# Kernel tuning notes

Measured on AMD Instinct MI355X. Metric: run time of the kernel, lower is better.

The kernel has to match this reference:

```python
import jax, jax.numpy as jnp
import numpy as np

B, S, D, V, L = 64, 2048, 256, 256, 4


def setup_inputs() -> dict:
    key = jax.random.key(0)
    ks = jax.random.split(key, 8)
    s = 1.0 / np.sqrt(D)  # PyTorch GRU init scale
    return {
        "x": jax.random.randint(ks[0], (B, S), 0, V, dtype=jnp.int32),
        "emb": jax.random.normal(ks[1], (V, D), jnp.float32) * 0.02,
        "W_ih": jax.random.uniform(ks[2], (L, 3 * D, D), jnp.float32, -s, s),
        "W_hh": jax.random.uniform(ks[3], (L, 3 * D, D), jnp.float32, -s, s),
        "b_ih": jax.random.uniform(ks[4], (L, 3 * D), jnp.float32, -s, s),
        "b_hh": jax.random.uniform(ks[5], (L, 3 * D), jnp.float32, -s, s),
        "W_out": jax.random.uniform(ks[6], (V, D), jnp.float32, -s, s),
        "b_out": jax.random.uniform(ks[7], (V,), jnp.float32, -s, s),
    }


def _gru_layer(seq, Wi, Wh, bi, bh):
    # seq: [B, S, D]. Precompute input-side gates for all timesteps (one GEMM).
    gi_all = jnp.einsum("bsd,gd->bsg", seq, Wi) + bi  # [B, S, 3D]

    def step(h, gi):
        gh = h @ Wh.T + bh  # [B, 3D]
        i_r, i_z, i_n = jnp.split(gi, 3, axis=-1)
        h_r, h_z, h_n = jnp.split(gh, 3, axis=-1)
        r = jax.nn.sigmoid(i_r + h_r)
        z = jax.nn.sigmoid(i_z + h_z)
        n = jnp.tanh(i_n + r * h_n)
        h_new = (1.0 - z) * n + z * h
        return h_new, h_new

    h0 = jnp.zeros((seq.shape[0], Wh.shape[1]), seq.dtype)
    _, out_t = jax.lax.scan(step, h0, jnp.swapaxes(gi_all, 0, 1))  # [S, B, D]
    return jnp.swapaxes(out_t, 0, 1)


def reference(x, emb, W_ih, W_hh, b_ih, b_hh, W_out, b_out):
    seq = emb[x]  # [B, S, D] embedding gather
    for l in range(W_ih.shape[0]):  # fixed small layer loop
        seq = _gru_layer(seq, W_ih[l], W_hh[l], b_ih[l], b_hh[l])
    logits = jnp.einsum("bsd,vd->bsv", seq, W_out) + b_out  # [B, S, V]
    return logits
```

## Files before the change

### kernel.cpp

```cpp
#include <hip/hip_runtime.h>
#include <hip/hip_bf16.h>


#define B_ 64
#define S_ 2048
#define D_ 256
#define V_ 256
#define L_ 4

typedef short  s16x8 __attribute__((ext_vector_type(8)));
typedef float  f32x4 __attribute__((ext_vector_type(4)));

static __device__ __forceinline__ unsigned short f2b(float f){
  union { float f; unsigned int u; } v; v.f = f;
  unsigned int u = v.u;
  return (unsigned short)((u + 0x7FFFu + ((u >> 16) & 1u)) >> 16);
}
static __device__ __forceinline__ float b2f_lo(unsigned int u){
  union { unsigned int u; float f; } v; v.u = u << 16; return v.f;
}
static __device__ __forceinline__ float b2f_hi(unsigned int u){
  union { unsigned int u; float f; } v; v.u = u & 0xffff0000u; return v.f;
}

static __device__ __forceinline__ void lds_load16(void* lds, const void* g){
  __builtin_amdgcn_global_load_lds(
      (const __attribute__((address_space(1))) unsigned int*)g,
      (__attribute__((address_space(3))) unsigned int*)lds, 16, 0, 0);
}

__global__ void cast_bf16_kernel(const float* __restrict__ src,
                                 unsigned short* __restrict__ dst, int n){
  int i = blockIdx.x * 256 + threadIdx.x;
  if (i < n) dst[i] = f2b(src[i]);
}

__global__ void embed_kernel(const int* __restrict__ x, const float* __restrict__ emb,
                             unsigned short* __restrict__ seq){
  int bs = blockIdx.x;
  int d  = threadIdx.x;
  int tok = x[bs];
  seq[(size_t)bs * D_ + d] = f2b(emb[tok * D_ + d]);
}

template<int OUTF32>
__global__ __launch_bounds__(256) void gemm_bt(const unsigned short* __restrict__ A,
                                               const unsigned short* __restrict__ Bw,
                                               const float* __restrict__ bias,
                                               void* __restrict__ Cp,
                                               int M, int N, int K, int ldc){
  __shared__ __align__(16) unsigned short As[128 * 32];
  __shared__ __align__(16) unsigned short Bs[128 * 32];
  const int tid = threadIdx.x, lane = tid & 63, w = tid >> 6;
  const int col = lane & 15, q = lane >> 4;
  const int m0 = blockIdx.x * 128, n0 = blockIdx.y * 128;
  const int mW = (w & 1) * 64, nW = (w >> 1) * 64;
  const size_t rowb = (size_t)K * 2;

  f32x4 acc[4][4] = {};

  for (int k0 = 0; k0 < K; k0 += 32){
    __syncthreads();
    #pragma unroll
    for (int inst = 0; inst < 2; ++inst){
      int c = inst * 256 + w * 64 + lane;
      int row = c >> 2, c16 = c & 3;
      lds_load16((char*)As + (inst * 4096 + w * 1024),
                 (const char*)A  + (size_t)(m0 + row) * rowb + (size_t)k0 * 2 + c16 * 16);
      lds_load16((char*)Bs + (inst * 4096 + w * 1024),
                 (const char*)Bw + (size_t)(n0 + row) * rowb + (size_t)k0 * 2 + c16 * 16);
    }
    __syncthreads();
    s16x8 aF[4], bF[4];
    #pragma unroll
    for (int t = 0; t < 4; ++t){
      aF[t] = *(const s16x8*)&As[(mW + t * 16 + col) * 32 + q * 8];
      bF[t] = *(const s16x8*)&Bs[(nW + t * 16 + col) * 32 + q * 8];
    }
    #pragma unroll
    for (int mi = 0; mi < 4; ++mi)
      #pragma unroll
      for (int ni = 0; ni < 4; ++ni)
        acc[mi][ni] = __builtin_amdgcn_mfma_f32_16x16x32_bf16(aF[mi], bF[ni], acc[mi][ni], 0, 0, 0);
  }

  float bn[4];
  #pragma unroll
  for (int ni = 0; ni < 4; ++ni) bn[ni] = bias[n0 + nW + ni * 16 + col];

  if (OUTF32){
    #pragma unroll
    for (int mi = 0; mi < 4; ++mi)
      #pragma unroll
      for (int ni = 0; ni < 4; ++ni)
        #pragma unroll
        for (int i = 0; i < 4; ++i){
          int r  = m0 + mW + mi * 16 + 4 * q + i;
          int cN = n0 + nW + ni * 16 + col;
          ((float*)Cp)[(size_t)r * ldc + cN] = acc[mi][ni][i] + bn[ni];
        }
  } else {
    const int b     = m0 >> 11;
    const int bi    = b >> 2;
    const int qs    = b & 3;
    const int sbase = (m0 & 2047) + mW;
    #pragma unroll
    for (int mi = 0; mi < 4; ++mi)
      #pragma unroll
      for (int ni = 0; ni < 4; ++ni)
        #pragma unroll
        for (int i = 0; i < 4; ++i){
          int s  = sbase + mi * 16 + 4 * q + i;
          int cN = n0 + nW + ni * 16 + col;
          int g  = cN >> 8, d = cN & 255;
          int lane_s = (d >> 5) * 64 + qs * 16 + (d & 15);
          int j  = ((d >> 4) & 1) * 3 + g;
          float v = acc[mi][ni][i] + bn[ni];
          size_t us = ((size_t)((bi * 2048 + s) * 3 + (j >> 1)) * 512 + lane_s) * 2 + (j & 1);
          ((unsigned short*)Cp)[us] = f2b(v);
        }
  }
}

__global__ __launch_bounds__(512, 2) void gru_scan(const unsigned int* __restrict__ gi32,
                                                   const unsigned short* __restrict__ Wh,
                                                   const float* __restrict__ bh,
                                                   unsigned short* __restrict__ outp){
  __shared__ __align__(16) unsigned short hb[2][4096];
  const int tid = threadIdx.x, lane = tid & 63, w = tid >> 6;
  const int col = lane & 15, q = lane >> 4;
  const int bi = blockIdx.x;
  const int dbase = w * 32;

  s16x8 bw[6][8];
  float bhv[6];
  #pragma unroll
  for (int g = 0; g < 3; ++g)
    #pragma unroll
    for (int t2 = 0; t2 < 2; ++t2){
      int gcol = g * 256 + dbase + t2 * 16 + col;
      bhv[g * 2 + t2] = bh[gcol];
      #pragma unroll
      for (int kk = 0; kk < 8; ++kk)
        bw[g * 2 + t2][kk] = *(const s16x8*)(Wh + gcol * 256 + kk * 32 + q * 8);
    }

  for (int i = tid; i < 4096; i += 512){ hb[0][i] = 0; hb[1][i] = 0; }

  float hprev[2] = {0.f, 0.f};
  const size_t obase = (size_t)(bi * 4 + q) * (S_ * D_) + dbase + col;

  const unsigned int* gp = gi32 + (size_t)bi * (S_ * 1536) + (w * 64 + lane);
  unsigned int cA0 = gp[0], cA1 = gp[512], cA2 = gp[1024];

  __syncthreads();

  auto step = [&](const unsigned short* hcur, unsigned short* hnxt,
                  unsigned int c0, unsigned int c1, unsigned int c2, int sidx){
    f32x4 acc[6];
    #pragma unroll
    for (int t = 0; t < 6; ++t){ f32x4 vv = {bhv[t], bhv[t], bhv[t], bhv[t]}; acc[t] = vv; }
    s16x8 a0 = *(const s16x8*)&hcur[lane * 8];
    #pragma unroll
    for (int kk = 0; kk < 8; ++kk){
      s16x8 aN = a0;
      if (kk < 7) aN = *(const s16x8*)&hcur[(kk + 1) * 512 + lane * 8];
      #pragma unroll
      for (int t = 0; t < 6; ++t)
        acc[t] = __builtin_amdgcn_mfma_f32_16x16x32_bf16(a0, bw[t][kk], acc[t], 0, 0, 0);
      a0 = aN;
    }
    float giR[2] = { b2f_lo(c0), b2f_hi(c1) };
    float giZ[2] = { b2f_hi(c0), b2f_lo(c2) };
    float giN[2] = { b2f_lo(c1), b2f_hi(c2) };
    #pragma unroll
    for (int t2 = 0; t2 < 2; ++t2){
      const int d = dbase + t2 * 16 + col;
      float pr = acc[t2][0]     + giR[t2];
      float pz = acc[2 + t2][0] + giZ[t2];
      float rg = __builtin_amdgcn_rcpf(1.f + __expf(-pr));
      float zg = __builtin_amdgcn_rcpf(1.f + __expf(-pz));
      float na = giN[t2] + rg * acc[4 + t2][0];
      float e2 = __expf(2.f * na);
      float ng = 1.f - 2.f * __builtin_amdgcn_rcpf(e2 + 1.f);
      float hn = ng + zg * (hprev[t2] - ng);
      hprev[t2] = hn;
      unsigned short hbits = f2b(hn);
      outp[obase + (size_t)sidx * D_ + t2 * 16] = hbits;
      hnxt[(d >> 5) * 512 + ((4 * q) + 16 * ((d >> 3) & 3)) * 8 + (d & 7)] = hbits;
    }
    asm volatile("s_waitcnt lgkmcnt(0)" ::: "memory");
    __builtin_amdgcn_s_barrier();
    asm volatile("" ::: "memory");
  };

  unsigned int cB0, cB1, cB2;
  for (int s = 0; s < S_; s += 2){
    cB0 = gp[1536]; cB1 = gp[1536 + 512]; cB2 = gp[1536 + 1024];
    step(hb[0], hb[1], cA0, cA1, cA2, s);
    const unsigned int* gpn = (s + 2 < S_) ? (gp + 3072) : gp;
    cA0 = gpn[0]; cA1 = gpn[512]; cA2 = gpn[1024];
    step(hb[1], hb[0], cB0, cB1, cB2, s + 1);
    gp += 3072;
  }
}

extern "C" void kernel_launch(void* const* d_in, const int* in_sizes, int n_in,
                              void* d_out, int out_size, void* d_ws, size_t ws_size,
                              hipStream_t stream){
  const int*   x    = (const int*)  d_in[0];
  const float* emb  = (const float*)d_in[1];
  const float* Wih  = (const float*)d_in[2];
  const float* Whh  = (const float*)d_in[3];
  const float* bih  = (const float*)d_in[4];
  const float* bhh  = (const float*)d_in[5];
  const float* Wout = (const float*)d_in[6];
  const float* bout = (const float*)d_in[7];
  float* out = (float*)d_out;

  char* ws = (char*)d_ws;
  unsigned short* seqA  = (unsigned short*)(ws);
  unsigned short* seqB  = (unsigned short*)(ws +  67108864);
  unsigned short* gibuf = (unsigned short*)(ws + 134217728);
  unsigned short* wihB  = (unsigned short*)(ws + 335544320);
  unsigned short* whhB  = (unsigned short*)(ws + 337117184);
  unsigned short* woutB = (unsigned short*)(ws + 338690048);

  cast_bf16_kernel<<<3072, 256, 0, stream>>>(Wih,  wihB,  L_ * 768 * 256);
  cast_bf16_kernel<<<3072, 256, 0, stream>>>(Whh,  whhB,  L_ * 768 * 256);
  cast_bf16_kernel<<< 256, 256, 0, stream>>>(Wout, woutB, V_ * D_);
  embed_kernel<<<B_ * S_, 256, 0, stream>>>(x, emb, seqA);

  const int M = B_ * S_;
  unsigned short* sIn = seqA;
  unsigned short* sOut = seqB;
  for (int l = 0; l < L_; ++l){
    gemm_bt<0><<<dim3(M / 128, 6), 256, 0, stream>>>(sIn, wihB + (size_t)l * 768 * 256,
                                                     bih + l * 768, gibuf, M, 768, 256, 768);
    gru_scan<<<16, 512, 0, stream>>>((const unsigned int*)gibuf,
                                     whhB + (size_t)l * 768 * 256, bhh + l * 768, sOut);
    unsigned short* t = sIn; sIn = sOut; sOut = t;
  }
  gemm_bt<1><<<dim3(M / 128, 2), 256, 0, stream>>>(sIn, woutB, bout, out, M, 256, 256, 256);
}
```

Measured before the change: 8.922 ms.

## Fuse all GRU layers into one persistent wavefront-pipelined kernel with flag sync

```diff
diff --git a/kernel.cpp b/kernel.cpp
--- a/kernel.cpp
+++ b/kernel.cpp
@@ -7,6 +7,11 @@
 #define D_ 256
 #define V_ 256
 #define L_ 4
+#define CHUNK_ 64
+#define NCHUNK_ 32
+#define LAG_ 2
+#define NWORK_ 192
+#define SLOTDW_ (16 * 64 * 1536)
 
 typedef short  s16x8 __attribute__((ext_vector_type(8)));
 typedef float  f32x4 __attribute__((ext_vector_type(4)));
@@ -27,6 +32,24 @@
   __builtin_amdgcn_global_load_lds(
       (const __attribute__((address_space(1))) unsigned int*)g,
       (__attribute__((address_space(3))) unsigned int*)lds, 16, 0, 0);
+}
+
+static __device__ __forceinline__ int aload(const int* p){
+  return __hip_atomic_load(p, __ATOMIC_RELAXED, __HIP_MEMORY_SCOPE_AGENT);
+}
+static __device__ __forceinline__ void spin_ge(const int* p, int tgt){
+  int n = 0;
+  while (aload(p) < tgt && n < 4000000){ __builtin_amdgcn_s_sleep(32); ++n; }
+}
+static __device__ __forceinline__ void spin_min16_ge(const int* p, int tgt){
+  int n = 0;
+  for (;;){
+    int m = 0x7fffffff;
+    #pragma unroll
+    for (int i = 0; i < 16; ++i) m = min(m, aload(p + i));
+    if (m >= tgt || n > 4000000) break;
+    __builtin_amdgcn_s_sleep(32); ++n;
+  }
 }
 
 __global__ void cast_bf16_kernel(const float* __restrict__ src,
@@ -43,12 +66,189 @@
   seq[(size_t)bs * D_ + d] = f2b(emb[tok * D_ + d]);
 }
 
-template<int OUTF32>
-__global__ __launch_bounds__(256) void gemm_bt(const unsigned short* __restrict__ A,
-                                               const unsigned short* __restrict__ Bw,
-                                               const float* __restrict__ bias,
-                                               void* __restrict__ Cp,
-                                               int M, int N, int K, int ldc){
+__global__ void init_flags_kernel(int* flags){
+  int i = threadIdx.x;
+  if (i < 192) flags[i] = 0;
+}
+
+__global__ __launch_bounds__(512, 2) void gru_pipe(
+    unsigned short* bufA, unsigned short* bufB,
+    unsigned int* ring,
+    const unsigned short* wih, const unsigned short* whh,
+    const float* bih, const float* bhh,
+    int* flags)
+{
+  __shared__ __align__(16) unsigned short smem[8192];
+  const int blk = blockIdx.x;
+  const int tid = threadIdx.x, lane = tid & 63, w = tid >> 6;
+  const int col = lane & 15, q = lane >> 4;
+  int* scanprog = flags;
+  int* jobdone  = flags + 64;
+
+  if (blk < 64){
+    const int l = blk >> 4, bi = blk & 15;
+    const unsigned short* Wh = whh + (size_t)l * 768 * 256;
+    const float* bh = bhh + l * 768;
+    unsigned short* outp = (l & 1) ? bufA : bufB;
+    const unsigned int* ringL = ring + (size_t)l * 2 * SLOTDW_;
+    const int dbase = w * 32;
+
+    s16x8 bw[6][8];
+    float bhv[6];
+    #pragma unroll
+    for (int g = 0; g < 3; ++g)
+      #pragma unroll
+      for (int t2 = 0; t2 < 2; ++t2){
+        int gcol = g * 256 + dbase + t2 * 16 + col;
+        bhv[g * 2 + t2] = bh[gcol];
+        #pragma unroll
+        for (int kk = 0; kk < 8; ++kk)
+          bw[g * 2 + t2][kk] = *(const s16x8*)(Wh + gcol * 256 + kk * 32 + q * 8);
+      }
+
+    unsigned short* hb0 = smem;
+    unsigned short* hb1 = smem + 4096;
+    for (int i = tid; i < 8192; i += 512) smem[i] = 0;
+
+    float hprev[2] = {0.f, 0.f};
+    const size_t obase = (size_t)(bi * 4 + q) * (S_ * D_) + dbase + col;
+    __syncthreads();
+
+    auto step = [&](const unsigned short* hcur, unsigned short* hnxt,
+                    unsigned int c0, unsigned int c1, unsigned int c2, int sidx){
+      f32x4 acc[6];
+      #pragma unroll
+      for (int t = 0; t < 6; ++t){ f32x4 vv = {bhv[t], bhv[t], bhv[t], bhv[t]}; acc[t] = vv; }
+      s16x8 a0 = *(const s16x8*)&hcur[lane * 8];
+      #pragma unroll
+      for (int kk = 0; kk < 8; ++kk){
+        s16x8 aN = a0;
+        if (kk < 7) aN = *(const s16x8*)&hcur[(kk + 1) * 512 + lane * 8];
+        #pragma unroll
+        for (int t = 0; t < 6; ++t)
+          acc[t] = __builtin_amdgcn_mfma_f32_16x16x32_bf16(a0, bw[t][kk], acc[t], 0, 0, 0);
+        a0 = aN;
+      }
+      float giR[2] = { b2f_lo(c0), b2f_hi(c1) };
+      float giZ[2] = { b2f_hi(c0), b2f_lo(c2) };
+      float giN[2] = { b2f_lo(c1), b2f_hi(c2) };
+      #pragma unroll
+      for (int t2 = 0; t2 < 2; ++t2){
+        const int d = dbase + t2 * 16 + col;
+        float pr = acc[t2][0]     + giR[t2];
+        float pz = acc[2 + t2][0] + giZ[t2];
+        float rg = __builtin_amdgcn_rcpf(1.f + __expf(-pr));
+        float zg = __builtin_amdgcn_rcpf(1.f + __expf(-pz));
+        float na = giN[t2] + rg * acc[4 + t2][0];
+        float e2 = __expf(2.f * na);
+        float ng = 1.f - 2.f * __builtin_amdgcn_rcpf(e2 + 1.f);
+        float hn = ng + zg * (hprev[t2] - ng);
+        hprev[t2] = hn;
+        unsigned short hbits = f2b(hn);
+        outp[obase + (size_t)sidx * D_ + t2 * 16] = hbits;
+        hnxt[(d >> 5) * 512 + ((4 * q) + 16 * ((d >> 3) & 3)) * 8 + (d & 7)] = hbits;
+      }
+      asm volatile("s_waitcnt lgkmcnt(0)" ::: "memory");
+      __builtin_amdgcn_s_barrier();
+      asm volatile("" ::: "memory");
+    };
+
+    for (int c = 0; c < NCHUNK_; ++c){
+      if (tid == 0) spin_ge(&jobdone[l * 32 + c], NWORK_);
+      __syncthreads();
+      __threadfence();
+      const unsigned int* gp = ringL + (size_t)(c & 1) * SLOTDW_ + bi * (64 * 1536) + (w * 64 + lane);
+      unsigned int cA0 = gp[0], cA1 = gp[512], cA2 = gp[1024];
+      const int sg0 = c * 64;
+      for (int s2 = 0; s2 < 64; s2 += 2){
+        const unsigned int* gq = gp + (size_t)(s2 + 1) * 1536;
+        unsigned int cB0 = gq[0], cB1 = gq[512], cB2 = gq[1024];
+        step(hb0, hb1, cA0, cA1, cA2, sg0 + s2);
+        const unsigned int* gr = gp + (size_t)((s2 + 2 < 64) ? s2 + 2 : s2) * 1536;
+        cA0 = gr[0]; cA1 = gr[512]; cA2 = gr[1024];
+        step(hb1, hb0, cB0, cB1, cB2, sg0 + s2 + 1);
+      }
+      __syncthreads();
+      __threadfence();
+      if (tid == 0)
+        __hip_atomic_store(&scanprog[l * 16 + bi], c + 1, __ATOMIC_RELAXED, __HIP_MEMORY_SCOPE_AGENT);
+    }
+  } else {
+    const int W = blk - 64, jm = W / 6, jn = W % 6;
+    unsigned short* As = smem;
+    unsigned short* Bs = smem + 4096;
+    const int mW = (w & 1) * 64, nW = (w >> 1) * 32;
+    const int rr = tid >> 2, c16 = tid & 3;
+
+    for (int T = 0; T <= NCHUNK_ - 1 + 3 * LAG_; ++T){
+      for (int l = 0; l < 4; ++l){
+        const int c = T - l * LAG_;
+        if (c < 0 || c >= NCHUNK_) continue;
+        if (tid == 0){
+          spin_min16_ge(&scanprog[l * 16], c - 1);
+          if (l > 0) spin_min16_ge(&scanprog[(l - 1) * 16], c + 1);
+        }
+        __syncthreads();
+        __threadfence();
+
+        const unsigned short* inA = (l & 1) ? bufB : bufA;
+        const unsigned short* Bw  = wih + (size_t)l * 768 * 256;
+        const float* bias = bih + l * 768;
+        const unsigned short* Arow = inA
+            + ((size_t)(2 * jm + (rr >> 6)) * S_ + (size_t)c * 64 + (rr & 63)) * 256;
+        const unsigned short* Brow = Bw + (size_t)(jn * 128 + rr) * 256;
+
+        f32x4 acc[4][2] = {};
+        for (int k0 = 0; k0 < 256; k0 += 32){
+          __syncthreads();
+          lds_load16((char*)As + tid * 16, (const char*)Arow + k0 * 2 + c16 * 16);
+          lds_load16((char*)Bs + tid * 16, (const char*)Brow + k0 * 2 + c16 * 16);
+          __syncthreads();
+          s16x8 aF[4], bF[2];
+          #pragma unroll
+          for (int t = 0; t < 4; ++t) aF[t] = *(const s16x8*)&As[(mW + t * 16 + col) * 32 + q * 8];
+          #pragma unroll
+          for (int t = 0; t < 2; ++t) bF[t] = *(const s16x8*)&Bs[(nW + t * 16 + col) * 32 + q * 8];
+          #pragma unroll
+          for (int mi = 0; mi < 4; ++mi)
+            #pragma unroll
+            for (int ni = 0; ni < 2; ++ni)
+              acc[mi][ni] = __builtin_amdgcn_mfma_f32_16x16x32_bf16(aF[mi], bF[ni], acc[mi][ni], 0, 0, 0);
+        }
+        float bn[2];
+        #pragma unroll
+        for (int ni = 0; ni < 2; ++ni) bn[ni] = bias[jn * 128 + nW + ni * 16 + col];
+
+        const int b = 2 * jm + (mW >> 6), bi2 = b >> 2, qs = b & 3;
+        unsigned short* slotB = (unsigned short*)(ring + (size_t)(l * 2 + (c & 1)) * SLOTDW_);
+        #pragma unroll
+        for (int mi = 0; mi < 4; ++mi)
+          #pragma unroll
+          for (int ni = 0; ni < 2; ++ni)
+            #pragma unroll
+            for (int i = 0; i < 4; ++i){
+              int sL = mi * 16 + 4 * q + i;
+              int cN = jn * 128 + nW + ni * 16 + col;
+              int g = cN >> 8, d = cN & 255;
+              int lane_s = (d >> 5) * 64 + qs * 16 + (d & 15);
+              int j = ((d >> 4) & 1) * 3 + g;
+              slotB[(((size_t)(bi2 * 64 + sL) * 3 + (j >> 1)) * 512 + lane_s) * 2 + (j & 1)]
+                  = f2b(acc[mi][ni][i] + bn[ni]);
+            }
+        __syncthreads();
+        __threadfence();
+        if (tid == 0)
+          __hip_atomic_fetch_add(&jobdone[l * 32 + c], 1, __ATOMIC_RELAXED, __HIP_MEMORY_SCOPE_AGENT);
+      }
+    }
+  }
+}
+
+__global__ __launch_bounds__(256) void gemm_out(const unsigned short* __restrict__ A,
+                                                const unsigned short* __restrict__ Bw,
+                                                const float* __restrict__ bias,
+                                                float* __restrict__ C,
+                                                int M, int N, int K, int ldc){
   __shared__ __align__(16) unsigned short As[128 * 32];
   __shared__ __align__(16) unsigned short Bs[128 * 32];
   const int tid = threadIdx.x, lane = tid & 63, w = tid >> 6;
@@ -58,7 +258,6 @@
   const size_t rowb = (size_t)K * 2;
 
   f32x4 acc[4][4] = {};
-
   for (int k0 = 0; k0 < K; k0 += 32){
     __syncthreads();
     #pragma unroll
@@ -83,126 +282,19 @@
       for (int ni = 0; ni < 4; ++ni)
         acc[mi][ni] = __builtin_amdgcn_mfma_f32_16x16x32_bf16(aF[mi], bF[ni], acc[mi][ni], 0, 0, 0);
   }
-
   float bn[4];
   #pragma unroll
   for (int ni = 0; ni < 4; ++ni) bn[ni] = bias[n0 + nW + ni * 16 + col];
-
-  if (OUTF32){
-    #pragma unroll
-    for (int mi = 0; mi < 4; ++mi)
-      #pragma unroll
-      for (int ni = 0; ni < 4; ++ni)
-        #pragma unroll
-        for (int i = 0; i < 4; ++i){
-          int r  = m0 + mW + mi * 16 + 4 * q + i;
-          int cN = n0 + nW + ni * 16 + col;
-          ((float*)Cp)[(size_t)r * ldc + cN] = acc[mi][ni][i] + bn[ni];
-        }
-  } else {
-    const int b     = m0 >> 11;
-    const int bi    = b >> 2;
-    const int qs    = b & 3;
-    const int sbase = (m0 & 2047) + mW;
-    #pragma unroll
-    for (int mi = 0; mi < 4; ++mi)
-      #pragma unroll
-      for (int ni = 0; ni < 4; ++ni)
-        #pragma unroll
-        for (int i = 0; i < 4; ++i){
-          int s  = sbase + mi * 16 + 4 * q + i;
-          int cN = n0 + nW + ni * 16 + col;
-          int g  = cN >> 8, d = cN & 255;
-          int lane_s = (d >> 5) * 64 + qs * 16 + (d & 15);
-          int j  = ((d >> 4) & 1) * 3 + g;
-          float v = acc[mi][ni][i] + bn[ni];
-          size_t us = ((size_t)((bi * 2048 + s) * 3 + (j >> 1)) * 512 + lane_s) * 2 + (j & 1);
-          ((unsigned short*)Cp)[us] = f2b(v);
-        }
-  }
-}
-
-__global__ __launch_bounds__(512, 2) void gru_scan(const unsigned int* __restrict__ gi32,
-                                                   const unsigned short* __restrict__ Wh,
-                                                   const float* __restrict__ bh,
-                                                   unsigned short* __restrict__ outp){
-  __shared__ __align__(16) unsigned short hb[2][4096];
-  const int tid = threadIdx.x, lane = tid & 63, w = tid >> 6;
-  const int col = lane & 15, q = lane >> 4;
-  const int bi = blockIdx.x;
-  const int dbase = w * 32;
-
-  s16x8 bw[6][8];
-  float bhv[6];
   #pragma unroll
-  for (int g = 0; g < 3; ++g)
-    #pragma unroll
-    for (int t2 = 0; t2 < 2; ++t2){
-      int gcol = g * 256 + dbase + t2 * 16 + col;
-      bhv[g * 2 + t2] = bh[gcol];
-      #pragma unroll
-      for (int kk = 0; kk < 8; ++kk)
-        bw[g * 2 + t2][kk] = *(const s16x8*)(Wh + gcol * 256 + kk * 32 + q * 8);
-    }
-
-  for (int i = tid; i < 4096; i += 512){ hb[0][i] = 0; hb[1][i] = 0; }
-
-  float hprev[2] = {0.f, 0.f};
-  const size_t obase = (size_t)(bi * 4 + q) * (S_ * D_) + dbase + col;
-
-  const unsigned int* gp = gi32 + (size_t)bi * (S_ * 1536) + (w * 64 + lane);
-  unsigned int cA0 = gp[0], cA1 = gp[512], cA2 = gp[1024];
-
-  __syncthreads();
-
-  auto step = [&](const unsigned short* hcur, unsigned short* hnxt,
-                  unsigned int c0, unsigned int c1, unsigned int c2, int sidx){
-    f32x4 acc[6];
-    #pragma unroll
-    for (int t = 0; t < 6; ++t){ f32x4 vv = {bhv[t], bhv[t], bhv[t], bhv[t]}; acc[t] = vv; }
-    s16x8 a0 = *(const s16x8*)&hcur[lane * 8];
-    #pragma unroll
-    for (int kk = 0; kk < 8; ++kk){
-      s16x8 aN = a0;
-      if (kk < 7) aN = *(const s16x8*)&hcur[(kk + 1) * 512 + lane * 8];
-      #pragma unroll
-      for (int t = 0; t < 6; ++t)
-        acc[t] = __builtin_amdgcn_mfma_f32_16x16x32_bf16(a0, bw[t][kk], acc[t], 0, 0, 0);
-      a0 = aN;
-    }
-    float giR[2] = { b2f_lo(c0), b2f_hi(c1) };
-    float giZ[2] = { b2f_hi(c0), b2f_lo(c2) };
-    float giN[2] = { b2f_lo(c1), b2f_hi(c2) };
-    #pragma unroll
-    for (int t2 = 0; t2 < 2; ++t2){
-      const int d = dbase + t2 * 16 + col;
-      float pr = acc[t2][0]     + giR[t2];
-      float pz = acc[2 + t2][0] + giZ[t2];
-      float rg = __builtin_amdgcn_rcpf(1.f + __expf(-pr));
-      float zg = __builtin_amdgcn_rcpf(1.f + __expf(-pz));
-      float na = giN[t2] + rg * acc[4 + t2][0];
-      float e2 = __expf(2.f * na);
-      float ng = 1.f - 2.f * __builtin_amdgcn_rcpf(e2 + 1.f);
-      float hn = ng + zg * (hprev[t2] - ng);
-      hprev[t2] = hn;
-      unsigned short hbits = f2b(hn);
-      outp[obase + (size_t)sidx * D_ + t2 * 16] = hbits;
-      hnxt[(d >> 5) * 512 + ((4 * q) + 16 * ((d >> 3) & 3)) * 8 + (d & 7)] = hbits;
-    }
-    asm volatile("s_waitcnt lgkmcnt(0)" ::: "memory");
-    __builtin_amdgcn_s_barrier();
-    asm volatile("" ::: "memory");
-  };
-
-  unsigned int cB0, cB1, cB2;
-  for (int s = 0; s < S_; s += 2){
-    cB0 = gp[1536]; cB1 = gp[1536 + 512]; cB2 = gp[1536 + 1024];
-    step(hb[0], hb[1], cA0, cA1, cA2, s);
-    const unsigned int* gpn = (s + 2 < S_) ? (gp + 3072) : gp;
-    cA0 = gpn[0]; cA1 = gpn[512]; cA2 = gpn[1024];
-    step(hb[1], hb[0], cB0, cB1, cB2, s + 1);
-    gp += 3072;
-  }
+  for (int mi = 0; mi < 4; ++mi)
+    #pragma unroll
+    for (int ni = 0; ni < 4; ++ni)
+      #pragma unroll
+      for (int i = 0; i < 4; ++i){
+        int r  = m0 + mW + mi * 16 + 4 * q + i;
+        int cN = n0 + nW + ni * 16 + col;
+        C[(size_t)r * ldc + cN] = acc[mi][ni][i] + bn[ni];
+      }
 }
 
 extern "C" void kernel_launch(void* const* d_in, const int* in_sizes, int n_in,
@@ -219,27 +311,22 @@
   float* out = (float*)d_out;
 
   char* ws = (char*)d_ws;
-  unsigned short* seqA  = (unsigned short*)(ws);
-  unsigned short* seqB  = (unsigned short*)(ws +  67108864);
-  unsigned short* gibuf = (unsigned short*)(ws + 134217728);
-  unsigned short* wihB  = (unsigned short*)(ws + 335544320);
-  unsigned short* whhB  = (unsigned short*)(ws + 337117184);
-  unsigned short* woutB = (unsigned short*)(ws + 338690048);
+  unsigned short* bufA  = (unsigned short*)(ws);
+  unsigned short* bufB  = (unsigned short*)(ws +  67108864);
+  unsigned int*   ring  = (unsigned int*)  (ws + 134217728);
+  unsigned short* wihB  = (unsigned short*)(ws + 184549376);
+  unsigned short* whhB  = (unsigned short*)(ws + 186122240);
+  unsigned short* woutB = (unsigned short*)(ws + 187695104);
+  int*            flags = (int*)           (ws + 187826176);
 
   cast_bf16_kernel<<<3072, 256, 0, stream>>>(Wih,  wihB,  L_ * 768 * 256);
   cast_bf16_kernel<<<3072, 256, 0, stream>>>(Whh,  whhB,  L_ * 768 * 256);
   cast_bf16_kernel<<< 256, 256, 0, stream>>>(Wout, woutB, V_ * D_);
-  embed_kernel<<<B_ * S_, 256, 0, stream>>>(x, emb, seqA);
-
-  const int M = B_ * S_;
-  unsigned short* sIn = seqA;
-  unsigned short* sOut = seqB;
-  for (int l = 0; l < L_; ++l){
-    gemm_bt<0><<<dim3(M / 128, 6), 256, 0, stream>>>(sIn, wihB + (size_t)l * 768 * 256,
-                                                     bih + l * 768, gibuf, M, 768, 256, 768);
-    gru_scan<<<16, 512, 0, stream>>>((const unsigned int*)gibuf,
-                                     whhB + (size_t)l * 768 * 256, bhh + l * 768, sOut);
-    unsigned short* t = sIn; sIn = sOut; sOut = t;
-  }
-  gemm_bt<1><<<dim3(M / 128, 2), 256, 0, stream>>>(sIn, woutB, bout, out, M, 256, 256, 256);
-}
+  embed_kernel<<<B_ * S_, 256, 0, stream>>>(x, emb, bufA);
+  init_flags_kernel<<<1, 256, 0, stream>>>(flags);
+
+  gru_pipe<<<256, 512, 0, stream>>>(bufA, bufB, ring, wihB, whhB, bih, bhh, flags);
+
+  gemm_out<<<dim3(B_ * S_ / 128, 2), 256, 0, stream>>>(bufA, woutB, bout, out,
+                                                       B_ * S_, 256, 256, 256);
+}
```

After: 26.83 ms. 201% more time.
